# Kernel tuning notes

Measured on AMD Instinct MI355X. Metric: run time of the kernel, lower is better.

Reference implementation:

```python
import jax, jax.numpy as jnp
import numpy as np

N_HEADS = 8
TOP_K = 2
EPS = 1e-5


def cross_node(x4, nf, tkv, Wq, bq, Wk, bk, Wv, bv, Wo, bo, gamma, beta, token_mask):
    # x4: [N, BL, 1, D]; nf: [N, BL, K, D]; tkv: [N, K, 1]; token_mask: [N] float (routed subset)
    N, BL, _, D = x4.shape
    K = nf.shape[2]
    H = N_HEADS
    dh = D // H
    nf = nf * tkv[:, None, :, :]  # use_weights: scale neighbors by topk similarity weights
    xf = x4.reshape(N * BL, D)
    nff = nf.reshape(N * BL, K, D)
    q = (xf @ Wq.T + bq).reshape(N * BL, H, dh)
    k = (nff @ Wk.T + bk).reshape(N * BL, K, H, dh)
    v = (nff @ Wv.T + bv).reshape(N * BL, K, H, dh)
    # flash_attn_func math: scaled dot-product over the K neighbors, per head
    scores = jnp.einsum('thd,tkhd->thk', q, k) / jnp.sqrt(jnp.asarray(dh, xf.dtype))
    attn = jax.nn.softmax(scores, axis=-1)
    o = jnp.einsum('thk,tkhd->thd', attn, v).reshape(N * BL, D)
    o = o @ Wo.T + bo
    # masked BatchNorm1d (training-mode batch stats over ONLY the gathered/routed tokens,
    # matching torch where each expert sees just its subset)
    m = jnp.broadcast_to(token_mask[:, None], (N, BL)).reshape(-1, 1)
    cnt = jnp.maximum(m.sum(), 1.0)
    mean = (o * m).sum(0) / cnt
    var = (((o - mean) ** 2) * m).sum(0) / cnt
    o = (o - mean) / jnp.sqrt(var + EPS) * gamma + beta
    return (o + xf).reshape(N, BL, D)


def moe_forward(x, mm, topk_values, Wr, br, eWq, eWk, eWv, eWo, ebq, ebk, ebv, ebo,
                eGamma, eBeta, eW1, eb1, mWq, mWk, mWv, mWo, mbq, mbk, mbv, mbo,
                mGamma, mBeta, mW2, mb2, topk_indices, modality_index):
    N, B, L, D = x.shape
    BL = B * L
    K = topk_indices.shape[1]
    E = Wr.shape[0]
    Mn = mWq.shape[0]
    # neighbor gather: nf[n, b*l, k] = x[topk_indices[n, k], b, l]
    nf = jnp.transpose(x[topk_indices], (0, 2, 3, 1, 4)).reshape(N, BL, K, D)
    x4 = x.reshape(N, BL, 1, D)
    tkv = topk_values.reshape(N, K, 1)
    # router softmax gating
    gate = jax.nn.softmax(mm.reshape(N, D) @ Wr.T + br, axis=-1)  # [N, E]
    _, te = jax.lax.top_k(gate, TOP_K)
    routed = jax.nn.one_hot(te, E, dtype=gate.dtype).sum(1)  # [N, E] 0/1
    f_i = routed.sum(0) / N
    P_i = gate.sum(0) / N
    balance_loss = E * jnp.sum(f_i * P_i)
    # capacity limiting via running cumsum per expert column
    keep = jnp.cumsum(routed, axis=0) <= (N / E)
    rprobs = gate * jnp.where(keep, routed, jnp.zeros_like(routed))
    active = rprobs.sum(-1) > 0  # [N]
    eprobs, eidx = jax.lax.top_k(rprobs, TOP_K)  # [N, TOP_K]
    # expert dispatch/combine (dense-masked equivalent of the per-expert gather/scatter)
    out_tok = jnp.zeros((N, BL, D), x.dtype)
    for i in range(E):
        sel = (eidx == i).any(-1) & active  # tokens gathered for expert i
        mask_f = sel.astype(x.dtype)
        prob_i = (eprobs * (eidx == i)).sum(-1)  # combine weight (0 for capacity-dropped)
        co = cross_node(x4, nf, tkv, eWq[i], ebq[i], eWk[i], ebk[i], eWv[i], ebv[i],
                        eWo[i], ebo[i], eGamma[i], eBeta[i], mask_f)
        co = co @ eW1[i].T + eb1[i]
        out_tok = out_tok + (mask_f * prob_i)[:, None, None] * co
    # modality experts: every token with modality m goes through modality expert m
    mod_out = jnp.zeros_like(out_tok)
    for m in range(Mn):
        mask_f = (modality_index[:, m, :] == 1).any(-1).astype(x.dtype)
        co = cross_node(x4, nf, tkv, mWq[m], mbq[m], mWk[m], mbk[m], mWv[m], mbv[m],
                        mWo[m], mbo[m], mGamma[m], mBeta[m], mask_f)
        co = co @ mW2[m].T + mb2[m]
        mod_out = mod_out + mask_f[:, None, None] * co
    out = (out_tok + mod_out / Mn).reshape(N, B, L, D)
    return out, balance_loss


def setup_inputs():
    key = jax.random.key(0)
    ks = jax.random.split(key, 7)
    N, B, L, D, K, E, Mn = 1024, 2, 8, 128, 16, 4, 4
    s = 1.0 / float(np.sqrt(D))
    inp = {}
    inp['x'] = jax.random.normal(ks[0], (N, B, L, D), jnp.float32)
    inp['mm'] = jax.random.normal(ks[1], (N, 1, D), jnp.float32)
    inp['topk_values'] = jax.random.uniform(ks[2], (N, K), jnp.float32)
    inp['topk_indices'] = jax.random.randint(ks[3], (N, K), 0, N, dtype=jnp.int32)
    inp['modality_index'] = jax.nn.one_hot(
        jax.random.randint(ks[4], (N,), 0, Mn, dtype=jnp.int32), Mn, dtype=jnp.int32
    ).reshape(N, Mn, 1)
    inp['Wr'] = jax.random.normal(ks[5], (E, D), jnp.float32) * s
    inp['br'] = jnp.zeros((E,), jnp.float32)
    kk = jax.random.split(ks[6], 10)
    for j, nm in enumerate(['eWq', 'eWk', 'eWv', 'eWo', 'eW1']):
        inp[nm] = jax.random.normal(kk[j], (E, D, D), jnp.float32) * s
    for j, nm in enumerate(['mWq', 'mWk', 'mWv', 'mWo', 'mW2']):
        inp[nm] = jax.random.normal(kk[5 + j], (Mn, D, D), jnp.float32) * s
    for nm in ['ebq', 'ebk', 'ebv', 'ebo', 'eBeta', 'eb1']:
        inp[nm] = jnp.zeros((E, D), jnp.float32)
    for nm in ['mbq', 'mbk', 'mbv', 'mbo', 'mBeta', 'mb2']:
        inp[nm] = jnp.zeros((Mn, D), jnp.float32)
    inp['eGamma'] = jnp.ones((E, D), jnp.float32)
    inp['mGamma'] = jnp.ones((Mn, D), jnp.float32)
    return inp


def reference(x, mm, topk_values, topk_indices, modality_index, Wr, br,
              eWq, eWk, eWv, eWo, ebq, ebk, ebv, ebo, eGamma, eBeta, eW1, eb1,
              mWq, mWk, mWv, mWo, mbq, mbk, mbv, mbo, mGamma, mBeta, mW2, mb2):
    return moe_forward(x, mm, topk_values, Wr, br, eWq, eWk, eWv, eWo, ebq, ebk, ebv, ebo,
                       eGamma, eBeta, eW1, eb1, mWq, mWk, mWv, mWo, mbq, mbk, mbv, mbo,
                       mGamma, mBeta, mW2, mb2, topk_indices, modality_index)
```

## Files before the change

### kernel.cpp

```cpp
#include <hip/hip_runtime.h>

typedef unsigned short u16;
typedef unsigned int u32;
typedef short short8 __attribute__((ext_vector_type(8)));
typedef float f32x4 __attribute__((ext_vector_type(4)));

#define NTOK 1024
#define TT 16384
#define DD 128
#define EPSV 1e-5f
#define ST 2097152

__device__ __forceinline__ u16 f2bf(float f) {
    u32 u = __float_as_uint(f);
    u += 0x7fffu + ((u >> 16) & 1u);
    return (u16)(u >> 16);
}
__device__ __forceinline__ u32 pack2(u16 a, u16 b) { return (u32)a | ((u32)b << 16); }
__device__ __forceinline__ void up2(u32 w, float& lo, float& hi) {
    lo = __uint_as_float(w << 16);
    hi = __uint_as_float(w & 0xffff0000u);
}

__global__ __launch_bounds__(256) void k_cvt(const float* __restrict__ x, u16* __restrict__ xb) {
    int i = blockIdx.x * 256 + threadIdx.x;
    const float4* p = (const float4*)x + (size_t)i * 2;
    float4 a = p[0], b = p[1];
    uint4 o;
    o.x = pack2(f2bf(a.x), f2bf(a.y));
    o.y = pack2(f2bf(a.z), f2bf(a.w));
    o.z = pack2(f2bf(b.x), f2bf(b.y));
    o.w = pack2(f2bf(b.z), f2bf(b.w));
    *((uint4*)xb + i) = o;
}

__global__ __launch_bounds__(256) void k_cvtw(const float* __restrict__ eWq, const float* __restrict__ eWk,
        const float* __restrict__ eWv, const float* __restrict__ eWo, const float* __restrict__ eW1,
        const float* __restrict__ mWq, const float* __restrict__ mWk, const float* __restrict__ mWv,
        const float* __restrict__ mWo, const float* __restrict__ mW2, u16* __restrict__ Wb) {
    int i = blockIdx.x * 256 + threadIdx.x;
    int tns = i >> 13;
    int off = (i & 8191) * 8;
    const float* src;
    switch (tns) {
        case 0: src = eWq; break; case 1: src = eWk; break; case 2: src = eWv; break;
        case 3: src = eWo; break; case 4: src = eW1; break; case 5: src = mWq; break;
        case 6: src = mWk; break; case 7: src = mWv; break; case 8: src = mWo; break;
        default: src = mW2; break;
    }
    const float4* p = (const float4*)(src + off);
    float4 a = p[0], b = p[1];
    uint4 o;
    o.x = pack2(f2bf(a.x), f2bf(a.y));
    o.y = pack2(f2bf(a.z), f2bf(a.w));
    o.z = pack2(f2bf(b.x), f2bf(b.y));
    o.w = pack2(f2bf(b.z), f2bf(b.w));
    *(uint4*)(Wb + tns * 65536 + off) = o;
}

__global__ __launch_bounds__(256) void k_logits(const float* __restrict__ mm, const float* __restrict__ Wr,
                                                const float* __restrict__ br, float* __restrict__ logits) {
    int i = blockIdx.x * 256 + threadIdx.x;
    int n = i >> 2, e = i & 3;
    const float4* a = (const float4*)(mm + (size_t)n * DD);
    const float4* w = (const float4*)(Wr + (size_t)e * DD);
    float s = 0.f;
#pragma unroll
    for (int j = 0; j < 32; j++) {
        float4 av = a[j], wv = w[j];
        s += av.x * wv.x + av.y * wv.y + av.z * wv.z + av.w * wv.w;
    }
    logits[i] = s + br[e];
}

__global__ __launch_bounds__(1024) void k_route(const float* __restrict__ logits, const int* __restrict__ modix,
                                                float* __restrict__ mask8, float* __restrict__ comb8,
                                                float* __restrict__ cnt8, float* __restrict__ bnsum,
                                                float* __restrict__ bnsq, float* __restrict__ loss) {
    __shared__ int wsum[4][16];
    __shared__ float red[16];
    int n = threadIdx.x;
    if (n < 16) red[n] = 0.f;
    bnsum[n] = 0.f; bnsq[n] = 0.f;
    float g[4];
    float mx = -1e30f;
#pragma unroll
    for (int e = 0; e < 4; e++) { g[e] = logits[n * 4 + e]; mx = fmaxf(mx, g[e]); }
    float s = 0.f;
#pragma unroll
    for (int e = 0; e < 4; e++) { g[e] = expf(g[e] - mx); s += g[e]; }
    float inv = 1.f / s;
#pragma unroll
    for (int e = 0; e < 4; e++) g[e] *= inv;
    int i0 = 0; float b0 = g[0];
#pragma unroll
    for (int e = 1; e < 4; e++) if (g[e] > b0) { b0 = g[e]; i0 = e; }
    int i1 = -1; float b1v = -1e30f;
#pragma unroll
    for (int e = 0; e < 4; e++) if (e != i0 && g[e] > b1v) { b1v = g[e]; i1 = e; }
    u32 rbits = (1u << i0) | (1u << i1);
    int wav = n >> 6, lane = n & 63;
    unsigned long long lm = (~0ull) >> (63 - lane);
    int pre[4];
#pragma unroll
    for (int e = 0; e < 4; e++) {
        unsigned long long m = __ballot((rbits >> e) & 1u);
        pre[e] = __popcll(m & lm);
        if (lane == 63) wsum[e][wav] = __popcll(m);
    }
    __syncthreads();
    float rp[4]; float rsum = 0.f;
#pragma unroll
    for (int e = 0; e < 4; e++) {
        int off = 0;
        for (int w = 0; w < 16; w++) if (w < wav) off += wsum[e][w];
        bool keep = (off + pre[e]) <= 256;
        rp[e] = (((rbits >> e) & 1u) && keep) ? g[e] : 0.f;
        rsum += rp[e];
    }
    bool active = rsum > 0.f;
    int j0 = 0; float c0 = rp[0];
#pragma unroll
    for (int e = 1; e < 4; e++) if (rp[e] > c0) { c0 = rp[e]; j0 = e; }
    int j1 = -1; float c1 = -1e30f;
#pragma unroll
    for (int e = 0; e < 4; e++) if (e != j0 && rp[e] > c1) { c1 = rp[e]; j1 = e; }
    float vals[16];
#pragma unroll
    for (int e = 0; e < 4; e++) {
        bool sel = active && (e == j0 || e == j1);
        float mf = sel ? 1.f : 0.f;
        mask8[e * NTOK + n] = mf;
        comb8[e * NTOK + n] = rp[e];
        vals[e] = mf;
    }
#pragma unroll
    for (int m = 0; m < 4; m++) {
        float mf = (modix[n * 4 + m] == 1) ? 1.f : 0.f;
        mask8[(4 + m) * NTOK + n] = mf;
        comb8[(4 + m) * NTOK + n] = 0.25f * mf;
        vals[4 + m] = mf;
    }
#pragma unroll
    for (int e = 0; e < 4; e++) vals[8 + e] = ((rbits >> e) & 1u) ? 1.f : 0.f;
#pragma unroll
    for (int e = 0; e < 4; e++) vals[12 + e] = g[e];
#pragma unroll
    for (int q = 0; q < 16; q++) {
        float v = vals[q];
        for (int off = 32; off; off >>= 1) v += __shfl_down(v, off, 64);
        if (lane == 0) atomicAdd(&red[q], v);
    }
    __syncthreads();
    if (n == 0) {
        for (int c = 0; c < 8; c++) cnt8[c] = fmaxf(16.f * red[c], 1.f);
        float l = 0.f;
        for (int e = 0; e < 4; e++) l += (red[8 + e] / 1024.f) * (red[12 + e] / 1024.f);
        loss[0] = 4.f * l;
    }
}

__global__ __launch_bounds__(256) void k_gemm_qkv(const u16* __restrict__ Xb, const u16* __restrict__ Wb,
        const float* __restrict__ ebq, const float* __restrict__ mbq,
        u16* __restrict__ Qb, u16* __restrict__ Kb, u16* __restrict__ Vb) {
    __shared__ u16 As[64 * 128];
    __shared__ u16 Bs[128 * 128];
    int tid = threadIdx.x; int bm = blockIdx.x; int c = blockIdx.y;
    int wq = (c < 4) ? c : 20 + (c - 4);
    int wk = (c < 4) ? 4 + c : 24 + (c - 4);
    int wv = (c < 4) ? 8 + c : 28 + (c - 4);
    const u16* Wsl[3] = { Wb + wq * 16384, Wb + wk * 16384, Wb + wv * 16384 };
    const float* bq = (c < 4) ? (ebq + c * 128) : (mbq + (c - 4) * 128);
    u16* Os[3] = { Qb + (size_t)c * ST, Kb + (size_t)c * ST, Vb + (size_t)c * ST };

    const uint4* asrc = (const uint4*)(Xb + (size_t)bm * 8192);
#pragma unroll
    for (int it = 0; it < 4; ++it) {
        int ci = it * 256 + tid;
        uint4 v = asrc[ci];
        int byte = ci * 16; int row = byte >> 8;
        *(uint4*)((char*)As + (byte ^ ((row & 7) << 4))) = v;
    }
    __syncthreads();
    int lane = tid & 63, wid = tid >> 6, lr = lane & 15, lg = lane >> 4;
    short8 a[4];
#pragma unroll
    for (int ks = 0; ks < 4; ++ks) {
        int kk = ks * 64 + lg * 16;
        int arow = wid * 16 + lr;
        a[ks] = *(const short8*)((const char*)As + ((arow * 256 + kk) ^ ((arow & 7) << 4)));
    }
    for (int y = 0; y < 3; ++y) {
        const uint4* wsrc = (const uint4*)Wsl[y];
#pragma unroll
        for (int it = 0; it < 8; ++it) {
            int qi = it * 256 + tid;
            uint4 v = wsrc[qi];
            int eo = qi * 8; int row = eo >> 7; int byte = eo * 2;
            *(uint4*)((char*)Bs + (byte ^ ((row & 7) << 4))) = v;
        }
        __syncthreads();
        f32x4 acc[8] = {};
#pragma unroll
        for (int ks = 0; ks < 4; ++ks) {
            int kk = ks * 64 + lg * 16;
#pragma unroll
            for (int nc = 0; nc < 8; ++nc) {
                int brow = nc * 16 + lr;
                short8 b = *(const short8*)((const char*)Bs + ((brow * 256 + kk) ^ ((brow & 7) << 4)));
                acc[nc] = __builtin_amdgcn_mfma_f32_16x16x32_bf16(a[ks], b, acc[nc], 0, 0, 0);
            }
        }
        int row0 = bm * 64 + wid * 16 + lg * 4;
        u16* Op = Os[y];
        bool hasb = (y == 0);
#pragma unroll
        for (int nc = 0; nc < 8; ++nc) {
            int col = nc * 16 + lr;
            float bb = hasb ? bq[col] : 0.f;
#pragma unroll
            for (int r = 0; r < 4; r++)
                Op[(size_t)(row0 + r) * 128 + col] = f2bf(acc[nc][r] + bb);
        }
        __syncthreads();
    }
}

__global__ __launch_bounds__(256) void k_attn(const u16* Qb, const u16* __restrict__ Kb,
        const u16* __restrict__ Vb, const float* __restrict__ tkv, const int* __restrict__ idx,
        const float* __restrict__ ebk, const float* __restrict__ ebv,
        const float* __restrict__ mbk, const float* __restrict__ mbv,
        const float* __restrict__ mask8, u16* Ob) {
    int bid = blockIdx.x;
    int c = bid & 7, inner = bid >> 3;
    int tid = threadIdx.x;
    int gid = inner * 256 + tid;
    int t = gid >> 3, h = gid & 7, n = t >> 4, bl = t & 15;
    if (mask8[c * NTOK + n] == 0.f) return;
    const u16* Qc = Qb + (size_t)c * ST;
    const u16* Kc = Kb + (size_t)c * ST;
    const u16* Vc = Vb + (size_t)c * ST;
    u16* Oc = Ob + (size_t)c * ST;
    const float* bk = (c < 4) ? (ebk + c * 128) : (mbk + (c - 4) * 128);
    const float* bv = (c < 4) ? (ebv + c * 128) : (mbv + (c - 4) * 128);
    float qv[16];
    {
        const uint4* qp = (const uint4*)(Qc + (size_t)t * 128 + h * 16);
        uint4 a = qp[0], b = qp[1];
        up2(a.x, qv[0], qv[1]);   up2(a.y, qv[2], qv[3]);
        up2(a.z, qv[4], qv[5]);   up2(a.w, qv[6], qv[7]);
        up2(b.x, qv[8], qv[9]);   up2(b.y, qv[10], qv[11]);
        up2(b.z, qv[12], qv[13]); up2(b.w, qv[14], qv[15]);
    }
    float qb = 0.f;
#pragma unroll
    for (int i = 0; i < 16; i++) qb += qv[i] * bk[h * 16 + i];
    int gsav[16]; float tsav[16];
#pragma unroll
    for (int k = 0; k < 16; k++) { gsav[k] = idx[n * 16 + k]; tsav[k] = tkv[n * 16 + k]; }
    float scv[16]; float smax = -1e30f;
    for (int k = 0; k < 16; k++) {
        const uint4* kp = (const uint4*)(Kc + (size_t)(gsav[k] * 16 + bl) * 128 + h * 16);
        uint4 a = kp[0], b = kp[1];
        float d0 = 0.f, d1 = 0.f, lo, hi;
        up2(a.x, lo, hi); d0 = fmaf(lo, qv[0], d0);  d1 = fmaf(hi, qv[1], d1);
        up2(a.y, lo, hi); d0 = fmaf(lo, qv[2], d0);  d1 = fmaf(hi, qv[3], d1);
        up2(a.z, lo, hi); d0 = fmaf(lo, qv[4], d0);  d1 = fmaf(hi, qv[5], d1);
        up2(a.w, lo, hi); d0 = fmaf(lo, qv[6], d0);  d1 = fmaf(hi, qv[7], d1);
        up2(b.x, lo, hi); d0 = fmaf(lo, qv[8], d0);  d1 = fmaf(hi, qv[9], d1);
        up2(b.y, lo, hi); d0 = fmaf(lo, qv[10], d0); d1 = fmaf(hi, qv[11], d1);
        up2(b.z, lo, hi); d0 = fmaf(lo, qv[12], d0); d1 = fmaf(hi, qv[13], d1);
        up2(b.w, lo, hi); d0 = fmaf(lo, qv[14], d0); d1 = fmaf(hi, qv[15], d1);
        float sv = 0.25f * (tsav[k] * (d0 + d1) + qb);
        scv[k] = sv; smax = fmaxf(smax, sv);
    }
    float sum = 0.f;
#pragma unroll
    for (int k = 0; k < 16; k++) { scv[k] = expf(scv[k] - smax); sum += scv[k]; }
    float inv = 1.f / sum;
    float o[16];
#pragma unroll
    for (int i = 0; i < 16; i++) o[i] = 0.f;
    for (int k = 0; k < 16; k++) {
        const uint4* vp = (const uint4*)(Vc + (size_t)(gsav[k] * 16 + bl) * 128 + h * 16);
        uint4 a = vp[0], b = vp[1];
        float cc = scv[k] * inv * tsav[k];
        float lo, hi;
        up2(a.x, lo, hi); o[0] = fmaf(lo, cc, o[0]);   o[1] = fmaf(hi, cc, o[1]);
        up2(a.y, lo, hi); o[2] = fmaf(lo, cc, o[2]);   o[3] = fmaf(hi, cc, o[3]);
        up2(a.z, lo, hi); o[4] = fmaf(lo, cc, o[4]);   o[5] = fmaf(hi, cc, o[5]);
        up2(a.w, lo, hi); o[6] = fmaf(lo, cc, o[6]);   o[7] = fmaf(hi, cc, o[7]);
        up2(b.x, lo, hi); o[8] = fmaf(lo, cc, o[8]);   o[9] = fmaf(hi, cc, o[9]);
        up2(b.y, lo, hi); o[10] = fmaf(lo, cc, o[10]); o[11] = fmaf(hi, cc, o[11]);
        up2(b.z, lo, hi); o[12] = fmaf(lo, cc, o[12]); o[13] = fmaf(hi, cc, o[13]);
        up2(b.w, lo, hi); o[14] = fmaf(lo, cc, o[14]); o[15] = fmaf(hi, cc, o[15]);
    }
#pragma unroll
    for (int i = 0; i < 16; i++) o[i] += bv[h * 16 + i];
    uint4 s0, s1;
    s0.x = pack2(f2bf(o[0]), f2bf(o[1]));  s0.y = pack2(f2bf(o[2]), f2bf(o[3]));
    s0.z = pack2(f2bf(o[4]), f2bf(o[5]));  s0.w = pack2(f2bf(o[6]), f2bf(o[7]));
    s1.x = pack2(f2bf(o[8]), f2bf(o[9]));  s1.y = pack2(f2bf(o[10]), f2bf(o[11]));
    s1.z = pack2(f2bf(o[12]), f2bf(o[13])); s1.w = pack2(f2bf(o[14]), f2bf(o[15]));
    uint4* op = (uint4*)(Oc + (size_t)t * 128 + h * 16);
    op[0] = s0; op[1] = s1;
}

__global__ __launch_bounds__(256) void k_gemm_o(const u16* __restrict__ Ab, const u16* __restrict__ Wb,
        const float* __restrict__ ebo, const float* __restrict__ mbo,
        u16* __restrict__ O2, const float* __restrict__ mask8,
        float* __restrict__ bnsum, float* __restrict__ bnsq) {
    __shared__ u16 As[64 * 128];
    __shared__ u16 Bs[128 * 128];
    __shared__ float ssum[128], ssq[128];
    int tid = threadIdx.x; int bm = blockIdx.x; int c = blockIdx.y;
    const float* maskp = mask8 + c * NTOK;
    if (maskp[bm * 4] == 0.f && maskp[bm * 4 + 1] == 0.f &&
        maskp[bm * 4 + 2] == 0.f && maskp[bm * 4 + 3] == 0.f) return;
    int wo = (c < 4) ? 12 + c : 32 + (c - 4);
    const u16* Wp = Wb + wo * 16384;
    const float* bo = (c < 4) ? (ebo + c * 128) : (mbo + (c - 4) * 128);
    if (tid < 128) { ssum[tid] = 0.f; ssq[tid] = 0.f; }
    const uint4* asrc = (const uint4*)(Ab + (size_t)c * ST + (size_t)bm * 8192);
#pragma unroll
    for (int it = 0; it < 4; ++it) {
        int ci = it * 256 + tid;
        uint4 v = asrc[ci];
        int byte = ci * 16; int row = byte >> 8;
        *(uint4*)((char*)As + (byte ^ ((row & 7) << 4))) = v;
    }
    const uint4* wsrc = (const uint4*)Wp;
#pragma unroll
    for (int it = 0; it < 8; ++it) {
        int qi = it * 256 + tid;
        uint4 v = wsrc[qi];
        int eo = qi * 8; int row = eo >> 7; int byte = eo * 2;
        *(uint4*)((char*)Bs + (byte ^ ((row & 7) << 4))) = v;
    }
    __syncthreads();
    int lane = tid & 63, wid = tid >> 6, lr = lane & 15, lg = lane >> 4;
    f32x4 acc[8] = {};
#pragma unroll
    for (int ks = 0; ks < 4; ++ks) {
        int kk = ks * 64 + lg * 16;
        int arow = wid * 16 + lr;
        short8 a = *(const short8*)((const char*)As + ((arow * 256 + kk) ^ ((arow & 7) << 4)));
#pragma unroll
        for (int nc = 0; nc < 8; ++nc) {
            int brow = nc * 16 + lr;
            short8 b = *(const short8*)((const char*)Bs + ((brow * 256 + kk) ^ ((brow & 7) << 4)));
            acc[nc] = __builtin_amdgcn_mfma_f32_16x16x32_bf16(a, b, acc[nc], 0, 0, 0);
        }
    }
    int nidx = bm * 4 + wid;
    float mk = maskp[nidx];
    int row0 = bm * 64 + wid * 16 + lg * 4;
    u16* O2c = O2 + (size_t)c * ST;
    float ps[8], pq[8];
#pragma unroll
    for (int nc = 0; nc < 8; ++nc) {
        int col = nc * 16 + lr;
        float bb = bo[col];
        float sv = 0.f, qv = 0.f;
#pragma unroll
        for (int r = 0; r < 4; r++) {
            float v = acc[nc][r] + bb;
            if (mk != 0.f) O2c[(size_t)(row0 + r) * 128 + col] = f2bf(v);
            sv += v; qv += v * v;
        }
        ps[nc] = sv * mk; pq[nc] = qv * mk;
    }
#pragma unroll
    for (int nc = 0; nc < 8; ++nc) {
        ps[nc] += __shfl_xor(ps[nc], 16, 64); ps[nc] += __shfl_xor(ps[nc], 32, 64);
        pq[nc] += __shfl_xor(pq[nc], 16, 64); pq[nc] += __shfl_xor(pq[nc], 32, 64);
    }
    if (lane < 16) {
#pragma unroll
        for (int nc = 0; nc < 8; ++nc) {
            atomicAdd(&ssum[nc * 16 + lane], ps[nc]);
            atomicAdd(&ssq[nc * 16 + lane], pq[nc]);
        }
    }
    __syncthreads();
    if (tid < 128) { atomicAdd(&bnsum[c * 128 + tid], ssum[tid]); atomicAdd(&bnsq[c * 128 + tid], ssq[tid]); }
}

__global__ __launch_bounds__(256) void k_gemm_w1(const u16* __restrict__ O2, const u16* __restrict__ Xb,
        const u16* __restrict__ Wb, const float* __restrict__ eb1, const float* __restrict__ mb2,
        const float* __restrict__ eGamma, const float* __restrict__ mGamma,
        const float* __restrict__ eBeta, const float* __restrict__ mBeta,
        const float* __restrict__ comb8, const float* __restrict__ cnt8,
        const float* __restrict__ bnsum, const float* __restrict__ bnsq,
        float* __restrict__ out) {
    __shared__ u16 As[64 * 128];
    __shared__ u16 Bs[128 * 128];
    __shared__ float scall[8][128], shall[8][128];
    int tid = threadIdx.x; int bm = blockIdx.x;
#pragma unroll
    for (int j = 0; j < 4; ++j) {
        int id = j * 256 + tid;
        int c = id >> 7, d = id & 127;
        float cnt = cnt8[c];
        float mean = bnsum[c * 128 + d] / cnt;
        float var = bnsq[c * 128 + d] / cnt - mean * mean;
        float rs = rsqrtf(var + EPSV);
        const float* ga = (c < 4) ? (eGamma + c * 128) : (mGamma + (c - 4) * 128);
        const float* be = (c < 4) ? (eBeta + c * 128) : (mBeta + (c - 4) * 128);
        float gg = ga[d];
        scall[c][d] = rs * gg;
        shall[c][d] = be[d] - mean * rs * gg;
    }
    __syncthreads();
    int lane = tid & 63, wid = tid >> 6, lr = lane & 15, lg = lane >> 4;
    f32x4 acc[8] = {};
    const uint4* xsrc = (const uint4*)(Xb + (size_t)bm * 8192);
    for (int c = 0; c < 8; ++c) {
        float wc4[4];
        wc4[0] = comb8[c * NTOK + bm * 4];     wc4[1] = comb8[c * NTOK + bm * 4 + 1];
        wc4[2] = comb8[c * NTOK + bm * 4 + 2]; wc4[3] = comb8[c * NTOK + bm * 4 + 3];
        if (wc4[0] == 0.f && wc4[1] == 0.f && wc4[2] == 0.f && wc4[3] == 0.f) continue;
        int wsl = (c < 4) ? 16 + c : 36 + (c - 4);
        const u16* Wp = Wb + wsl * 16384;
        const uint4* osrc = (const uint4*)(O2 + (size_t)c * ST + (size_t)bm * 8192);
#pragma unroll
        for (int it = 0; it < 4; ++it) {
            int qi = it * 256 + tid;
            int eo = qi * 8; int row = eo >> 7; int cb = eo & 127;
            float wc = wc4[it];
            uint4 ov = osrc[qi]; uint4 xv = xsrc[qi];
            float olo, ohi, xlo, xhi;
            uint4 hh;
            up2(ov.x, olo, ohi); up2(xv.x, xlo, xhi);
            hh.x = pack2(f2bf((olo * scall[c][cb] + shall[c][cb] + xlo) * wc),
                         f2bf((ohi * scall[c][cb + 1] + shall[c][cb + 1] + xhi) * wc));
            up2(ov.y, olo, ohi); up2(xv.y, xlo, xhi);
            hh.y = pack2(f2bf((olo * scall[c][cb + 2] + shall[c][cb + 2] + xlo) * wc),
                         f2bf((ohi * scall[c][cb + 3] + shall[c][cb + 3] + xhi) * wc));
            up2(ov.z, olo, ohi); up2(xv.z, xlo, xhi);
            hh.z = pack2(f2bf((olo * scall[c][cb + 4] + shall[c][cb + 4] + xlo) * wc),
                         f2bf((ohi * scall[c][cb + 5] + shall[c][cb + 5] + xhi) * wc));
            up2(ov.w, olo, ohi); up2(xv.w, xlo, xhi);
            hh.w = pack2(f2bf((olo * scall[c][cb + 6] + shall[c][cb + 6] + xlo) * wc),
                         f2bf((ohi * scall[c][cb + 7] + shall[c][cb + 7] + xhi) * wc));
            *(uint4*)((char*)As + ((eo * 2) ^ ((row & 7) << 4))) = hh;
        }
        const uint4* wsrc = (const uint4*)Wp;
#pragma unroll
        for (int it = 0; it < 8; ++it) {
            int qi = it * 256 + tid;
            uint4 v = wsrc[qi];
            int eo = qi * 8; int row = eo >> 7; int byte = eo * 2;
            *(uint4*)((char*)Bs + (byte ^ ((row & 7) << 4))) = v;
        }
        __syncthreads();
#pragma unroll
        for (int ks = 0; ks < 4; ++ks) {
            int kk = ks * 64 + lg * 16;
            int arow = wid * 16 + lr;
            short8 a = *(const short8*)((const char*)As + ((arow * 256 + kk) ^ ((arow & 7) << 4)));
#pragma unroll
            for (int nc = 0; nc < 8; ++nc) {
                int brow = nc * 16 + lr;
                short8 b = *(const short8*)((const char*)Bs + ((brow * 256 + kk) ^ ((brow & 7) << 4)));
                acc[nc] = __builtin_amdgcn_mfma_f32_16x16x32_bf16(a, b, acc[nc], 0, 0, 0);
            }
        }
        __syncthreads();
    }
    int nidx = bm * 4 + wid;
    int row0 = bm * 64 + wid * 16 + lg * 4;
    float wc8[8];
#pragma unroll
    for (int c = 0; c < 8; ++c) wc8[c] = comb8[c * NTOK + nidx];
#pragma unroll
    for (int nc = 0; nc < 8; ++nc) {
        int col = nc * 16 + lr;
        float bias = 0.f;
#pragma unroll
        for (int c = 0; c < 8; ++c) {
            const float* b1 = (c < 4) ? (eb1 + c * 128) : (mb2 + (c - 4) * 128);
            bias += wc8[c] * b1[col];
        }
#pragma unroll
        for (int r = 0; r < 4; r++)
            out[(size_t)(row0 + r) * 128 + col] = acc[nc][r] + bias;
    }
}

extern "C" void kernel_launch(void* const* d_in, const int* in_sizes, int n_in,
                              void* d_out, int out_size, void* d_ws, size_t ws_size,
                              hipStream_t stream) {
    (void)in_sizes; (void)n_in; (void)ws_size; (void)out_size;
    const float* x    = (const float*)d_in[0];
    const float* mm   = (const float*)d_in[1];
    const float* tkv  = (const float*)d_in[2];
    const int*   idx  = (const int*)d_in[3];
    const int*   modi = (const int*)d_in[4];
    const float* Wr   = (const float*)d_in[5];
    const float* br   = (const float*)d_in[6];
    const float* eWq = (const float*)d_in[7],  *eWk = (const float*)d_in[8],  *eWv = (const float*)d_in[9];
    const float* eWo = (const float*)d_in[10], *eW1 = (const float*)d_in[11];
    const float* mWq = (const float*)d_in[12], *mWk = (const float*)d_in[13], *mWv = (const float*)d_in[14];
    const float* mWo = (const float*)d_in[15], *mW2 = (const float*)d_in[16];
    const float* ebq = (const float*)d_in[17], *ebk = (const float*)d_in[18], *ebv = (const float*)d_in[19];
    const float* ebo = (const float*)d_in[20], *eBeta = (const float*)d_in[21], *eb1 = (const float*)d_in[22];
    const float* mbq = (const float*)d_in[23], *mbk = (const float*)d_in[24], *mbv = (const float*)d_in[25];
    const float* mbo = (const float*)d_in[26], *mBeta = (const float*)d_in[27], *mb2 = (const float*)d_in[28];
    const float* eGamma = (const float*)d_in[29], *mGamma = (const float*)d_in[30];
    float* out = (float*)d_out;

    char* wsb = (char*)d_ws;
    const size_t MB = 1024 * 1024;
    u16* Xb = (u16*)wsb;
    u16* Wb = (u16*)(wsb + 4 * MB);
    u16* Qb = (u16*)(wsb + 8 * MB);
    u16* Kb = (u16*)(wsb + 40 * MB);
    u16* Vb = (u16*)(wsb + 72 * MB);
    u16* O2 = (u16*)(wsb + 104 * MB);
    float* logits = (float*)(wsb + 136 * MB);
    float* comb8 = logits + 4096;
    float* mask8 = comb8 + 8192;
    float* cnt8  = mask8 + 8192;
    float* bnsum = cnt8 + 16;
    float* bnsq  = bnsum + 1024;

    k_cvt<<<1024, 256, 0, stream>>>(x, Xb);
    k_cvtw<<<320, 256, 0, stream>>>(eWq, eWk, eWv, eWo, eW1, mWq, mWk, mWv, mWo, mW2, Wb);
    k_logits<<<16, 256, 0, stream>>>(mm, Wr, br, logits);
    k_route<<<1, 1024, 0, stream>>>(logits, modi, mask8, comb8, cnt8, bnsum, bnsq,
                                    out + (size_t)TT * DD);
    k_gemm_qkv<<<dim3(256, 8), 256, 0, stream>>>(Xb, Wb, ebq, mbq, Qb, Kb, Vb);
    k_attn<<<4096, 256, 0, stream>>>(Qb, Kb, Vb, tkv, idx, ebk, ebv, mbk, mbv, mask8, Qb);
    k_gemm_o<<<dim3(256, 8), 256, 0, stream>>>(Qb, Wb, ebo, mbo, O2, mask8, bnsum, bnsq);
    k_gemm_w1<<<256, 256, 0, stream>>>(O2, Xb, Wb, eb1, mb2, eGamma, mGamma, eBeta, mBeta,
                                       comb8, cnt8, bnsum, bnsq, out);
}
```

Baseline: 131.0 us.

## Fuse prep kernels, skip inactive Q projections, widen final GEMM to 512 threads

Merges the x conversion, weight conversion and router-logit kernels into one launch to cut launch overhead. The QKV GEMM now skips the Q projection for 64-row tiles where none of the four tokens is routed to that expert, since attention never reads those rows. The attention kernel makes the token index wave-uniform via readfirstlane and partially unrolls the K/V loops. The final W1 GEMM moves to 512 threads with a 4x2 warp split so each warp holds fewer accumulators, which may raise occupancy but adds shared-memory traffic per tile.

```diff
diff --git a/kernel.cpp b/kernel.cpp
--- a/kernel.cpp
+++ b/kernel.cpp
@@ -22,55 +22,56 @@
     hi = __uint_as_float(w & 0xffff0000u);
 }
 
-__global__ __launch_bounds__(256) void k_cvt(const float* __restrict__ x, u16* __restrict__ xb) {
-    int i = blockIdx.x * 256 + threadIdx.x;
-    const float4* p = (const float4*)x + (size_t)i * 2;
-    float4 a = p[0], b = p[1];
-    uint4 o;
-    o.x = pack2(f2bf(a.x), f2bf(a.y));
-    o.y = pack2(f2bf(a.z), f2bf(a.w));
-    o.z = pack2(f2bf(b.x), f2bf(b.y));
-    o.w = pack2(f2bf(b.z), f2bf(b.w));
-    *((uint4*)xb + i) = o;
-}
-
-__global__ __launch_bounds__(256) void k_cvtw(const float* __restrict__ eWq, const float* __restrict__ eWk,
+__global__ __launch_bounds__(256) void k_prep(const float* __restrict__ x,
+        const float* __restrict__ eWq, const float* __restrict__ eWk,
         const float* __restrict__ eWv, const float* __restrict__ eWo, const float* __restrict__ eW1,
         const float* __restrict__ mWq, const float* __restrict__ mWk, const float* __restrict__ mWv,
-        const float* __restrict__ mWo, const float* __restrict__ mW2, u16* __restrict__ Wb) {
-    int i = blockIdx.x * 256 + threadIdx.x;
-    int tns = i >> 13;
-    int off = (i & 8191) * 8;
-    const float* src;
-    switch (tns) {
-        case 0: src = eWq; break; case 1: src = eWk; break; case 2: src = eWv; break;
-        case 3: src = eWo; break; case 4: src = eW1; break; case 5: src = mWq; break;
-        case 6: src = mWk; break; case 7: src = mWv; break; case 8: src = mWo; break;
-        default: src = mW2; break;
-    }
-    const float4* p = (const float4*)(src + off);
-    float4 a = p[0], b = p[1];
-    uint4 o;
-    o.x = pack2(f2bf(a.x), f2bf(a.y));
-    o.y = pack2(f2bf(a.z), f2bf(a.w));
-    o.z = pack2(f2bf(b.x), f2bf(b.y));
-    o.w = pack2(f2bf(b.z), f2bf(b.w));
-    *(uint4*)(Wb + tns * 65536 + off) = o;
-}
-
-__global__ __launch_bounds__(256) void k_logits(const float* __restrict__ mm, const float* __restrict__ Wr,
-                                                const float* __restrict__ br, float* __restrict__ logits) {
-    int i = blockIdx.x * 256 + threadIdx.x;
-    int n = i >> 2, e = i & 3;
-    const float4* a = (const float4*)(mm + (size_t)n * DD);
-    const float4* w = (const float4*)(Wr + (size_t)e * DD);
-    float s = 0.f;
-#pragma unroll
-    for (int j = 0; j < 32; j++) {
-        float4 av = a[j], wv = w[j];
-        s += av.x * wv.x + av.y * wv.y + av.z * wv.z + av.w * wv.w;
-    }
-    logits[i] = s + br[e];
+        const float* __restrict__ mWo, const float* __restrict__ mW2,
+        const float* __restrict__ mm, const float* __restrict__ Wr, const float* __restrict__ br,
+        u16* __restrict__ Xb, u16* __restrict__ Wb, float* __restrict__ logits) {
+    int bid = blockIdx.x; int tid = threadIdx.x;
+    if (bid < 1024) {
+        int i = bid * 256 + tid;
+        const float4* p = (const float4*)x + (size_t)i * 2;
+        float4 a = p[0], b = p[1];
+        uint4 o;
+        o.x = pack2(f2bf(a.x), f2bf(a.y));
+        o.y = pack2(f2bf(a.z), f2bf(a.w));
+        o.z = pack2(f2bf(b.x), f2bf(b.y));
+        o.w = pack2(f2bf(b.z), f2bf(b.w));
+        *((uint4*)Xb + i) = o;
+    } else if (bid < 1344) {
+        int i = (bid - 1024) * 256 + tid;
+        int tns = i >> 13;
+        int off = (i & 8191) * 8;
+        const float* src;
+        switch (tns) {
+            case 0: src = eWq; break; case 1: src = eWk; break; case 2: src = eWv; break;
+            case 3: src = eWo; break; case 4: src = eW1; break; case 5: src = mWq; break;
+            case 6: src = mWk; break; case 7: src = mWv; break; case 8: src = mWo; break;
+            default: src = mW2; break;
+        }
+        const float4* p = (const float4*)(src + off);
+        float4 a = p[0], b = p[1];
+        uint4 o;
+        o.x = pack2(f2bf(a.x), f2bf(a.y));
+        o.y = pack2(f2bf(a.z), f2bf(a.w));
+        o.z = pack2(f2bf(b.x), f2bf(b.y));
+        o.w = pack2(f2bf(b.z), f2bf(b.w));
+        *(uint4*)(Wb + tns * 65536 + off) = o;
+    } else {
+        int i = (bid - 1344) * 256 + tid;
+        int n = i >> 2, e = i & 3;
+        const float4* a = (const float4*)(mm + (size_t)n * DD);
+        const float4* w = (const float4*)(Wr + (size_t)e * DD);
+        float s = 0.f;
+#pragma unroll
+        for (int j = 0; j < 32; j++) {
+            float4 av = a[j], wv = w[j];
+            s += av.x * wv.x + av.y * wv.y + av.z * wv.z + av.w * wv.w;
+        }
+        logits[i] = s + br[e];
+    }
 }
 
 __global__ __launch_bounds__(1024) void k_route(const float* __restrict__ logits, const int* __restrict__ modix,
@@ -162,6 +163,7 @@
 
 __global__ __launch_bounds__(256) void k_gemm_qkv(const u16* __restrict__ Xb, const u16* __restrict__ Wb,
         const float* __restrict__ ebq, const float* __restrict__ mbq,
+        const float* __restrict__ mask8,
         u16* __restrict__ Qb, u16* __restrict__ Kb, u16* __restrict__ Vb) {
     __shared__ u16 As[64 * 128];
     __shared__ u16 Bs[128 * 128];
@@ -172,6 +174,9 @@
     const u16* Wsl[3] = { Wb + wq * 16384, Wb + wk * 16384, Wb + wv * 16384 };
     const float* bq = (c < 4) ? (ebq + c * 128) : (mbq + (c - 4) * 128);
     u16* Os[3] = { Qb + (size_t)c * ST, Kb + (size_t)c * ST, Vb + (size_t)c * ST };
+    const float* maskp = mask8 + c * NTOK;
+    bool qact = (maskp[bm * 4] != 0.f) || (maskp[bm * 4 + 1] != 0.f) ||
+                (maskp[bm * 4 + 2] != 0.f) || (maskp[bm * 4 + 3] != 0.f);
 
     const uint4* asrc = (const uint4*)(Xb + (size_t)bm * 8192);
 #pragma unroll
@@ -191,6 +196,7 @@
         a[ks] = *(const short8*)((const char*)As + ((arow * 256 + kk) ^ ((arow & 7) << 4)));
     }
     for (int y = 0; y < 3; ++y) {
+        if (y == 0 && !qact) continue;
         const uint4* wsrc = (const uint4*)Wsl[y];
 #pragma unroll
         for (int it = 0; it < 8; ++it) {
@@ -235,7 +241,9 @@
     int c = bid & 7, inner = bid >> 3;
     int tid = threadIdx.x;
     int gid = inner * 256 + tid;
-    int t = gid >> 3, h = gid & 7, n = t >> 4, bl = t & 15;
+    int t = gid >> 3, h = gid & 7;
+    int n = __builtin_amdgcn_readfirstlane(t >> 4);
+    int bl = t & 15;
     if (mask8[c * NTOK + n] == 0.f) return;
     const u16* Qc = Qb + (size_t)c * ST;
     const u16* Kc = Kb + (size_t)c * ST;
@@ -259,6 +267,7 @@
 #pragma unroll
     for (int k = 0; k < 16; k++) { gsav[k] = idx[n * 16 + k]; tsav[k] = tkv[n * 16 + k]; }
     float scv[16]; float smax = -1e30f;
+#pragma unroll 2
     for (int k = 0; k < 16; k++) {
         const uint4* kp = (const uint4*)(Kc + (size_t)(gsav[k] * 16 + bl) * 128 + h * 16);
         uint4 a = kp[0], b = kp[1];
@@ -281,6 +290,7 @@
     float o[16];
 #pragma unroll
     for (int i = 0; i < 16; i++) o[i] = 0.f;
+#pragma unroll 2
     for (int k = 0; k < 16; k++) {
         const uint4* vp = (const uint4*)(Vc + (size_t)(gsav[k] * 16 + bl) * 128 + h * 16);
         uint4 a = vp[0], b = vp[1];
@@ -386,7 +396,7 @@
     if (tid < 128) { atomicAdd(&bnsum[c * 128 + tid], ssum[tid]); atomicAdd(&bnsq[c * 128 + tid], ssq[tid]); }
 }
 
-__global__ __launch_bounds__(256) void k_gemm_w1(const u16* __restrict__ O2, const u16* __restrict__ Xb,
+__global__ __launch_bounds__(512) void k_gemm_w1(const u16* __restrict__ O2, const u16* __restrict__ Xb,
         const u16* __restrict__ Wb, const float* __restrict__ eb1, const float* __restrict__ mb2,
         const float* __restrict__ eGamma, const float* __restrict__ mGamma,
         const float* __restrict__ eBeta, const float* __restrict__ mBeta,
@@ -398,8 +408,8 @@
     __shared__ float scall[8][128], shall[8][128];
     int tid = threadIdx.x; int bm = blockIdx.x;
 #pragma unroll
-    for (int j = 0; j < 4; ++j) {
-        int id = j * 256 + tid;
+    for (int j = 0; j < 2; ++j) {
+        int id = j * 512 + tid;
         int c = id >> 7, d = id & 127;
         float cnt = cnt8[c];
         float mean = bnsum[c * 128 + d] / cnt;
@@ -413,7 +423,8 @@
     }
     __syncthreads();
     int lane = tid & 63, wid = tid >> 6, lr = lane & 15, lg = lane >> 4;
-    f32x4 acc[8] = {};
+    int wm = wid & 3, wn = wid >> 2;
+    f32x4 acc[4] = {};
     const uint4* xsrc = (const uint4*)(Xb + (size_t)bm * 8192);
     for (int c = 0; c < 8; ++c) {
         float wc4[4];
@@ -424,10 +435,10 @@
         const u16* Wp = Wb + wsl * 16384;
         const uint4* osrc = (const uint4*)(O2 + (size_t)c * ST + (size_t)bm * 8192);
 #pragma unroll
-        for (int it = 0; it < 4; ++it) {
-            int qi = it * 256 + tid;
+        for (int it = 0; it < 2; ++it) {
+            int qi = it * 512 + tid;
             int eo = qi * 8; int row = eo >> 7; int cb = eo & 127;
-            float wc = wc4[it];
+            float wc = wc4[row >> 4];
             uint4 ov = osrc[qi]; uint4 xv = xsrc[qi];
             float olo, ohi, xlo, xhi;
             uint4 hh;
@@ -447,8 +458,8 @@
         }
         const uint4* wsrc = (const uint4*)Wp;
 #pragma unroll
-        for (int it = 0; it < 8; ++it) {
-            int qi = it * 256 + tid;
+        for (int it = 0; it < 4; ++it) {
+            int qi = it * 512 + tid;
             uint4 v = wsrc[qi];
             int eo = qi * 8; int row = eo >> 7; int byte = eo * 2;
             *(uint4*)((char*)Bs + (byte ^ ((row & 7) << 4))) = v;
@@ -457,25 +468,25 @@
 #pragma unroll
         for (int ks = 0; ks < 4; ++ks) {
             int kk = ks * 64 + lg * 16;
-            int arow = wid * 16 + lr;
+            int arow = wm * 16 + lr;
             short8 a = *(const short8*)((const char*)As + ((arow * 256 + kk) ^ ((arow & 7) << 4)));
 #pragma unroll
-            for (int nc = 0; nc < 8; ++nc) {
-                int brow = nc * 16 + lr;
+            for (int nc = 0; nc < 4; ++nc) {
+                int brow = wn * 64 + nc * 16 + lr;
                 short8 b = *(const short8*)((const char*)Bs + ((brow * 256 + kk) ^ ((brow & 7) << 4)));
                 acc[nc] = __builtin_amdgcn_mfma_f32_16x16x32_bf16(a, b, acc[nc], 0, 0, 0);
             }
         }
         __syncthreads();
     }
-    int nidx = bm * 4 + wid;
-    int row0 = bm * 64 + wid * 16 + lg * 4;
+    int nidx = bm * 4 + wm;
+    int row0 = bm * 64 + wm * 16 + lg * 4;
     float wc8[8];
 #pragma unroll
     for (int c = 0; c < 8; ++c) wc8[c] = comb8[c * NTOK + nidx];
 #pragma unroll
-    for (int nc = 0; nc < 8; ++nc) {
-        int col = nc * 16 + lr;
+    for (int nc = 0; nc < 4; ++nc) {
+        int col = wn * 64 + nc * 16 + lr;
         float bias = 0.f;
 #pragma unroll
         for (int c = 0; c < 8; ++c) {
@@ -525,14 +536,13 @@
     float* bnsum = cnt8 + 16;
     float* bnsq  = bnsum + 1024;
 
-    k_cvt<<<1024, 256, 0, stream>>>(x, Xb);
-    k_cvtw<<<320, 256, 0, stream>>>(eWq, eWk, eWv, eWo, eW1, mWq, mWk, mWv, mWo, mW2, Wb);
-    k_logits<<<16, 256, 0, stream>>>(mm, Wr, br, logits);
+    k_prep<<<1360, 256, 0, stream>>>(x, eWq, eWk, eWv, eWo, eW1, mWq, mWk, mWv, mWo, mW2,
+                                     mm, Wr, br, Xb, Wb, logits);
     k_route<<<1, 1024, 0, stream>>>(logits, modi, mask8, comb8, cnt8, bnsum, bnsq,
                                     out + (size_t)TT * DD);
-    k_gemm_qkv<<<dim3(256, 8), 256, 0, stream>>>(Xb, Wb, ebq, mbq, Qb, Kb, Vb);
+    k_gemm_qkv<<<dim3(256, 8), 256, 0, stream>>>(Xb, Wb, ebq, mbq, mask8, Qb, Kb, Vb);
     k_attn<<<4096, 256, 0, stream>>>(Qb, Kb, Vb, tkv, idx, ebk, ebv, mbk, mbv, mask8, Qb);
     k_gemm_o<<<dim3(256, 8), 256, 0, stream>>>(Qb, Wb, ebo, mbo, O2, mask8, bnsum, bnsq);
-    k_gemm_w1<<<256, 256, 0, stream>>>(O2, Xb, Wb, eb1, mb2, eGamma, mGamma, eBeta, mBeta,
+    k_gemm_w1<<<256, 512, 0, stream>>>(O2, Xb, Wb, eb1, mb2, eGamma, mGamma, eBeta, mBeta,
                                        comb8, cnt8, bnsum, bnsq, out);
 }
```

Result: faster. 119.0 us (-9.1%).
